# Performance work log

Measured on AMD Instinct MI355X. Metric: run time of the kernel, lower is better.

The kernel has to match this reference:

```python
import jax, jax.numpy as jnp
import numpy as np

N_NODES = 50000
N_EDGES = 1600000
NFEAT, NHID, NCLASS = 512, 128, 40


def setup_inputs() -> dict:
    key = jax.random.key(0)
    ks = jax.random.split(key, 10)
    x = jax.random.normal(ks[0], (N_NODES, NFEAT), dtype=jnp.float32)
    edge_src = jax.random.randint(ks[1], (N_EDGES,), 0, N_NODES, dtype=jnp.int32)
    edge_dst = jax.random.randint(ks[2], (N_EDGES,), 0, N_NODES, dtype=jnp.int32)
    edge_weight = jax.random.uniform(ks[3], (N_EDGES,), dtype=jnp.float32)
    # GraphConvolution params: gc1 (nfeat->nhid), one additional (nhid->nhid), gc2 (nhid->nclass)
    s1 = 1.0 / np.sqrt(NHID)
    s2 = 1.0 / np.sqrt(NCLASS)
    W1 = jax.random.uniform(ks[4], (NFEAT, NHID), minval=-s1, maxval=s1, dtype=jnp.float32)
    b1 = jax.random.uniform(ks[5], (NHID,), minval=-s1, maxval=s1, dtype=jnp.float32)
    Wh = jax.random.uniform(ks[6], (NHID, NHID), minval=-s1, maxval=s1, dtype=jnp.float32)
    bh = jax.random.uniform(ks[7], (NHID,), minval=-s1, maxval=s1, dtype=jnp.float32)
    W2 = jax.random.uniform(ks[8], (NHID, NCLASS), minval=-s2, maxval=s2, dtype=jnp.float32)
    b2 = jax.random.uniform(ks[9], (NCLASS,), minval=-s2, maxval=s2, dtype=jnp.float32)
    return {"x": x, "edge_src": edge_src, "edge_dst": edge_dst, "edge_weight": edge_weight,
            "W1": W1, "b1": b1, "Wh": Wh, "bh": bh, "W2": W2, "b2": b2}


def reference(x, edge_src, edge_dst, edge_weight, W1, b1, Wh, bh, W2, b2):
    def spmm(h):
        # out[i] = sum_j adj[i, j] * h[j]  with adj given as weighted edge list (src=j, dst=i)
        return jax.ops.segment_sum(edge_weight[:, None] * h[edge_src], edge_dst,
                                   num_segments=x.shape[0])

    def gconv(h, W, b):
        return spmm(h @ W) + b  # dense transform then sparse aggregation

    h = jax.nn.relu(gconv(x, W1, b1))       # gc1
    h = jax.nn.relu(gconv(h, Wh, bh))        # additional hidden layer
    h = gconv(h, W2, b2)                     # gc2
    return jax.nn.log_softmax(h, axis=1)
```

## Files before the change

### kernel.cpp

```cpp
#include <hip/hip_runtime.h>
#include <hip/hip_bf16.h>
#include <math.h>

#define N_NODES 50000
#define N_EDGES 1600000
#define NFEAT 512
#define NHID 128
#define NCLASS 40

#define NBUCKETS 196
#define BUCKET_CAP 16384

typedef __attribute__((ext_vector_type(8))) short bf16x8;
typedef __attribute__((ext_vector_type(4))) float f32x4;

static __device__ __forceinline__ float asfloat_u32(unsigned int u) {
    union { unsigned int u; float f; } c;
    c.u = u;
    return c.f;
}
static __device__ __forceinline__ unsigned int asu32_f(float f) {
    union { float f; unsigned int u; } c;
    c.f = f;
    return c.u;
}
static __device__ __forceinline__ unsigned short f2bf(float f) {
    union { float f; unsigned int u; } c;
    c.f = f;
    unsigned int r = c.u + 0x7FFFu + ((c.u >> 16) & 1u);
    return (unsigned short)(r >> 16);
}

__global__ __launch_bounds__(256) void prep_kernel(const float* __restrict__ W1,
                                                   unsigned short* __restrict__ Wt1,
                                                   const float* __restrict__ Wh,
                                                   unsigned short* __restrict__ Wth,
                                                   int* __restrict__ bucketCursor) {
    int idx = blockIdx.x * 256 + threadIdx.x;
    if (idx < NFEAT * NHID) {
        int k = idx >> 7;
        int n = idx & 127;
        Wt1[(size_t)n * NFEAT + k] = f2bf(W1[idx]);
    } else if (idx < NFEAT * NHID + NHID * NHID) {
        int j = idx - NFEAT * NHID;
        int k = j >> 7;
        int n = j & 127;
        Wth[(size_t)n * NHID + k] = f2bf(Wh[j]);
    } else {
        int j = idx - (NFEAT * NHID + NHID * NHID);
        if (j < NBUCKETS) bucketCursor[j] = j * BUCKET_CAP;
    }
}

#define LDP 40
#define GEMM_LDS_BYTES ((64 + 128) * LDP * 2)

template <bool A_IS_BF16>
static __device__ __forceinline__ void gemm64_body(const void* __restrict__ Ap,
                                                   const unsigned short* __restrict__ Wt,
                                                   unsigned short* __restrict__ C,
                                                   const int M, const int K,
                                                   char* smem, int bid) {
    unsigned short* As = (unsigned short*)smem;
    unsigned short* Bs = (unsigned short*)smem + 64 * LDP;
    const int tid = threadIdx.x;
    const int wave = tid >> 6;
    const int lane = tid & 63;
    const int ln = lane & 15;
    const int quad = lane >> 4;
    const int row0 = bid * 64;

    const int ar = tid >> 2;
    const int ac = (tid & 3) * 8;
    const bool arOk = (row0 + ar) < M;
    const int bn = tid >> 1;
    const int bk = (tid & 1) * 16;

    f32x4 acc[8];
#pragma unroll
    for (int t = 0; t < 8; ++t) acc[t] = (f32x4){0.f, 0.f, 0.f, 0.f};

    for (int kc = 0; kc < K; kc += 32) {
        bf16x8 va;
        if (A_IS_BF16) {
            if (arOk) {
                va = *(const bf16x8*)((const unsigned short*)Ap +
                                      (size_t)(row0 + ar) * K + kc + ac);
            } else {
#pragma unroll
                for (int i = 0; i < 8; ++i) va[i] = 0;
            }
        } else {
            if (arOk) {
                const float* Af = (const float*)Ap + (size_t)(row0 + ar) * K + kc + ac;
                float4 f0 = *(const float4*)(Af);
                float4 f1 = *(const float4*)(Af + 4);
                va[0] = (short)f2bf(f0.x); va[1] = (short)f2bf(f0.y);
                va[2] = (short)f2bf(f0.z); va[3] = (short)f2bf(f0.w);
                va[4] = (short)f2bf(f1.x); va[5] = (short)f2bf(f1.y);
                va[6] = (short)f2bf(f1.z); va[7] = (short)f2bf(f1.w);
            } else {
#pragma unroll
                for (int i = 0; i < 8; ++i) va[i] = 0;
            }
        }
        const unsigned short* Bg = Wt + (size_t)bn * K + kc + bk;
        bf16x8 vb0 = *(const bf16x8*)Bg;
        bf16x8 vb1 = *(const bf16x8*)(Bg + 8);

        __syncthreads();
        *(bf16x8*)&As[ar * LDP + ac] = va;
        *(bf16x8*)&Bs[bn * LDP + bk] = vb0;
        *(bf16x8*)&Bs[bn * LDP + bk + 8] = vb1;
        __syncthreads();

        bf16x8 a = *(const bf16x8*)&As[(wave * 16 + ln) * LDP + quad * 8];
#pragma unroll
        for (int t = 0; t < 8; ++t) {
            bf16x8 b = *(const bf16x8*)&Bs[(t * 16 + ln) * LDP + quad * 8];
            acc[t] = __builtin_amdgcn_mfma_f32_16x16x32_bf16(a, b, acc[t], 0, 0, 0);
        }
    }

#pragma unroll
    for (int t = 0; t < 8; ++t) {
#pragma unroll
        for (int r = 0; r < 4; ++r) {
            int row = row0 + wave * 16 + quad * 4 + r;
            if (row < M) C[(size_t)row * 128 + t * 16 + ln] = f2bf(acc[t][r]);
        }
    }
}

static __device__ __forceinline__ void bin_body(const int* __restrict__ src,
                                                const int* __restrict__ dst,
                                                const float* __restrict__ w,
                                                int* __restrict__ bucketCursor,
                                                uint2* __restrict__ binned,
                                                int n, char* smem, int bid) {
    int* hist = (int*)smem;
    int* cur = (int*)smem + NBUCKETS;
    const int tid = threadIdx.x;
    const int base = bid * 4096;
    if (tid < NBUCKETS) hist[tid] = 0;
    __syncthreads();
#pragma unroll
    for (int r = 0; r < 16; ++r) {
        int e = base + r * 256 + tid;
        if (e < n) atomicAdd(&hist[dst[e] >> 8], 1);
    }
    __syncthreads();
    if (tid < NBUCKETS && hist[tid] > 0)
        cur[tid] = atomicAdd(&bucketCursor[tid], hist[tid]);
    __syncthreads();
#pragma unroll
    for (int r = 0; r < 16; ++r) {
        int e = base + r * 256 + tid;
        if (e < n) {
            int d = dst[e];
            int pos = atomicAdd(&cur[d >> 8], 1);
            uint2 rec;
            rec.x = (unsigned int)src[e] | ((unsigned int)(d & 255) << 16);
            rec.y = asu32_f(w[e]);
            binned[pos] = rec;
        }
    }
}

#define GEMM1_BLOCKS 782
#define BIN_BLOCKS 391
__global__ __launch_bounds__(256) void fused_gemm1_bin(const float* __restrict__ x,
                                                       const unsigned short* __restrict__ Wt1,
                                                       unsigned short* __restrict__ tb,
                                                       const int* __restrict__ src,
                                                       const int* __restrict__ dst,
                                                       const float* __restrict__ w,
                                                       int* __restrict__ bucketCursor,
                                                       uint2* __restrict__ binned) {
    __shared__ char smem[GEMM_LDS_BYTES];
    if (blockIdx.x < GEMM1_BLOCKS) {
        gemm64_body<false>(x, Wt1, tb, N_NODES, NFEAT, smem, blockIdx.x);
    } else {
        bin_body(src, dst, w, bucketCursor, binned, N_EDGES, smem,
                 blockIdx.x - GEMM1_BLOCKS);
    }
}

__global__ __launch_bounds__(256) void gemm64_l2(const unsigned short* __restrict__ A,
                                                 const unsigned short* __restrict__ Wt,
                                                 unsigned short* __restrict__ C) {
    __shared__ char smem[GEMM_LDS_BYTES];
    gemm64_body<true>(A, Wt, C, N_NODES, NHID, smem, blockIdx.x);
}

__global__ __launch_bounds__(256) void build_csr(const uint2* __restrict__ binned,
                                                 const int* __restrict__ bucketCursor,
                                                 unsigned int* __restrict__ pairs,
                                                 int* __restrict__ row_ptr) {
    __shared__ int bs[256];
    __shared__ int hist[256];
    __shared__ int sc[256];
    __shared__ int cur[256];
    const int b = blockIdx.x;
    const int tid = threadIdx.x;

    int c = (tid < NBUCKETS) ? (bucketCursor[tid] - tid * BUCKET_CAP) : 0;
    bs[tid] = c;
    __syncthreads();
    for (int off = 1; off < 256; off <<= 1) {
        int t = (tid >= off) ? bs[tid - off] : 0;
        __syncthreads();
        bs[tid] += t;
        __syncthreads();
    }
    const int cnt = bucketCursor[b] - b * BUCKET_CAP;
    const int segStart = bs[b] - cnt;
    if (b == NBUCKETS - 1 && tid == 0) row_ptr[N_NODES] = bs[NBUCKETS - 1];
    const uint2* seg = binned + (size_t)b * BUCKET_CAP;

    hist[tid] = 0;
    __syncthreads();
    for (int i = tid; i < cnt; i += 256)
        atomicAdd(&hist[seg[i].x >> 16], 1);
    __syncthreads();
    int v = hist[tid];
    sc[tid] = v;
    __syncthreads();
    for (int off = 1; off < 256; off <<= 1) {
        int t = (tid >= off) ? sc[tid - off] : 0;
        __syncthreads();
        sc[tid] += t;
        __syncthreads();
    }
    int excl = sc[tid] - v;
    int node = b * 256 + tid;
    if (node < N_NODES) row_ptr[node] = segStart + excl;
    cur[tid] = segStart + excl;
    __syncthreads();
    for (int i = tid; i < cnt; i += 256) {
        uint2 p = seg[i];
        int pos = atomicAdd(&cur[p.x >> 16], 1);
        pairs[pos] = (p.x & 0xFFFFu) | ((unsigned int)f2bf(asfloat_u32(p.y)) << 16);
    }
}

__global__ __launch_bounds__(256) void gemm_n40_bf16A(const unsigned short* __restrict__ A,
                                                      const float* __restrict__ Bm,
                                                      unsigned short* __restrict__ C, int M) {
    __shared__ float As[64][132];
    __shared__ float Bs[128 * 40];
    const int tid = threadIdx.x;
    const int tr = tid >> 2;
    const int tc = tid & 3;
    const int row0 = blockIdx.x * 64;

#pragma unroll
    for (int q = tid; q < 2048; q += 256) {
        int r = q >> 5;
        int c = (q & 31) << 2;
        int row = row0 + r;
        uint2 u = make_uint2(0u, 0u);
        if (row < M) u = *(const uint2*)(A + (size_t)row * 128 + c);
        As[r][c + 0] = asfloat_u32(u.x << 16);
        As[r][c + 1] = asfloat_u32(u.x & 0xFFFF0000u);
        As[r][c + 2] = asfloat_u32(u.y << 16);
        As[r][c + 3] = asfloat_u32(u.y & 0xFFFF0000u);
    }
    for (int q = tid; q < 128 * 40; q += 256) Bs[q] = Bm[q];
    __syncthreads();

    float acc[10];
#pragma unroll
    for (int j = 0; j < 10; ++j) acc[j] = 0.f;

    for (int k = 0; k < 128; ++k) {
        float a = As[tr][k];
#pragma unroll
        for (int j = 0; j < 10; ++j) acc[j] += a * Bs[k * 40 + tc * 10 + j];
    }

    int row = row0 + tr;
    if (row < M) {
#pragma unroll
        for (int j = 0; j < 10; ++j) C[(size_t)row * 40 + tc * 10 + j] = f2bf(acc[j]);
    }
}

__global__ __launch_bounds__(256) void spmm_bias_relu_bf16(const unsigned short* __restrict__ t,
                                                           const int* __restrict__ row_ptr,
                                                           const unsigned int* __restrict__ pairs,
                                                           const float* __restrict__ bias,
                                                           unsigned short* __restrict__ out) {
    const int node = blockIdx.x * 4 + (threadIdx.x >> 6);
    const int lane = threadIdx.x & 63;
    const int e0 = row_ptr[node];
    const int e1 = row_ptr[node + 1];
    float ax = 0.f, ay = 0.f;
    int e = e0;
    for (; e + 8 <= e1; e += 8) {
        unsigned int p0 = pairs[e],     p1 = pairs[e + 1], p2 = pairs[e + 2], p3 = pairs[e + 3];
        unsigned int p4 = pairs[e + 4], p5 = pairs[e + 5], p6 = pairs[e + 6], p7 = pairs[e + 7];
        unsigned int v0 = *(const unsigned int*)(t + (size_t)(p0 & 0xFFFFu) * 128 + lane * 2);
        unsigned int v1 = *(const unsigned int*)(t + (size_t)(p1 & 0xFFFFu) * 128 + lane * 2);
        unsigned int v2 = *(const unsigned int*)(t + (size_t)(p2 & 0xFFFFu) * 128 + lane * 2);
        unsigned int v3 = *(const unsigned int*)(t + (size_t)(p3 & 0xFFFFu) * 128 + lane * 2);
        unsigned int v4 = *(const unsigned int*)(t + (size_t)(p4 & 0xFFFFu) * 128 + lane * 2);
        unsigned int v5 = *(const unsigned int*)(t + (size_t)(p5 & 0xFFFFu) * 128 + lane * 2);
        unsigned int v6 = *(const unsigned int*)(t + (size_t)(p6 & 0xFFFFu) * 128 + lane * 2);
        unsigned int v7 = *(const unsigned int*)(t + (size_t)(p7 & 0xFFFFu) * 128 + lane * 2);
        float w0 = asfloat_u32(p0 & 0xFFFF0000u), w1 = asfloat_u32(p1 & 0xFFFF0000u);
        float w2 = asfloat_u32(p2 & 0xFFFF0000u), w3 = asfloat_u32(p3 & 0xFFFF0000u);
        float w4 = asfloat_u32(p4 & 0xFFFF0000u), w5 = asfloat_u32(p5 & 0xFFFF0000u);
        float w6 = asfloat_u32(p6 & 0xFFFF0000u), w7 = asfloat_u32(p7 & 0xFFFF0000u);
        ax += w0 * asfloat_u32(v0 << 16); ay += w0 * asfloat_u32(v0 & 0xFFFF0000u);
        ax += w1 * asfloat_u32(v1 << 16); ay += w1 * asfloat_u32(v1 & 0xFFFF0000u);
        ax += w2 * asfloat_u32(v2 << 16); ay += w2 * asfloat_u32(v2 & 0xFFFF0000u);
        ax += w3 * asfloat_u32(v3 << 16); ay += w3 * asfloat_u32(v3 & 0xFFFF0000u);
        ax += w4 * asfloat_u32(v4 << 16); ay += w4 * asfloat_u32(v4 & 0xFFFF0000u);
        ax += w5 * asfloat_u32(v5 << 16); ay += w5 * asfloat_u32(v5 & 0xFFFF0000u);
        ax += w6 * asfloat_u32(v6 << 16); ay += w6 * asfloat_u32(v6 & 0xFFFF0000u);
        ax += w7 * asfloat_u32(v7 << 16); ay += w7 * asfloat_u32(v7 & 0xFFFF0000u);
    }
    for (; e < e1; ++e) {
        unsigned int p = pairs[e];
        float w = asfloat_u32(p & 0xFFFF0000u);
        unsigned int v = *(const unsigned int*)(t + (size_t)(p & 0xFFFFu) * 128 + lane * 2);
        ax += w * asfloat_u32(v << 16);
        ay += w * asfloat_u32(v & 0xFFFF0000u);
    }
    float2 b = *(const float2*)&bias[lane * 2];
    ax = fmaxf(ax + b.x, 0.f);
    ay = fmaxf(ay + b.y, 0.f);
    unsigned int packed = ((unsigned int)f2bf(ax)) | (((unsigned int)f2bf(ay)) << 16);
    *(unsigned int*)(out + (size_t)node * 128 + lane * 2) = packed;
}

__global__ __launch_bounds__(256) void spmm_logsoftmax(const unsigned short* __restrict__ t,
                                                       const int* __restrict__ row_ptr,
                                                       const unsigned int* __restrict__ pairs,
                                                       const float* __restrict__ bias,
                                                       float* __restrict__ out) {
    const int node = blockIdx.x * 4 + (threadIdx.x >> 6);
    const int lane = threadIdx.x & 63;
    const int e0 = row_ptr[node];
    const int e1 = row_ptr[node + 1];
    const bool act = lane < NCLASS;
    float acc = 0.f;
    int e = e0;
    for (; e + 4 <= e1; e += 4) {
        unsigned int p0 = pairs[e], p1 = pairs[e + 1], p2 = pairs[e + 2], p3 = pairs[e + 3];
        if (act) {
            float v0 = asfloat_u32((unsigned int)t[(size_t)(p0 & 0xFFFFu) * NCLASS + lane] << 16);
            float v1 = asfloat_u32((unsigned int)t[(size_t)(p1 & 0xFFFFu) * NCLASS + lane] << 16);
            float v2 = asfloat_u32((unsigned int)t[(size_t)(p2 & 0xFFFFu) * NCLASS + lane] << 16);
            float v3 = asfloat_u32((unsigned int)t[(size_t)(p3 & 0xFFFFu) * NCLASS + lane] << 16);
            acc += asfloat_u32(p0 & 0xFFFF0000u) * v0 + asfloat_u32(p1 & 0xFFFF0000u) * v1 +
                   asfloat_u32(p2 & 0xFFFF0000u) * v2 + asfloat_u32(p3 & 0xFFFF0000u) * v3;
        }
    }
    for (; e < e1; ++e) {
        unsigned int p = pairs[e];
        if (act)
            acc += asfloat_u32(p & 0xFFFF0000u) *
                   asfloat_u32((unsigned int)t[(size_t)(p & 0xFFFFu) * NCLASS + lane] << 16);
    }
    float logit = act ? (acc + bias[lane]) : -INFINITY;
    float m = logit;
#pragma unroll
    for (int off = 32; off; off >>= 1) m = fmaxf(m, __shfl_xor(m, off));
    float ex = act ? __expf(logit - m) : 0.f;
    float ssum = ex;
#pragma unroll
    for (int off = 32; off; off >>= 1) ssum += __shfl_xor(ssum, off);
    if (act) out[(size_t)node * NCLASS + lane] = logit - m - __logf(ssum);
}


extern "C" void kernel_launch(void* const* d_in, const int* in_sizes, int n_in,
                              void* d_out, int out_size, void* d_ws, size_t ws_size,
                              hipStream_t stream) {
    const float* x = (const float*)d_in[0];
    const int* edge_src = (const int*)d_in[1];
    const int* edge_dst = (const int*)d_in[2];
    const float* edge_weight = (const float*)d_in[3];
    const float* W1 = (const float*)d_in[4];
    const float* b1 = (const float*)d_in[5];
    const float* Wh = (const float*)d_in[6];
    const float* bh = (const float*)d_in[7];
    const float* W2 = (const float*)d_in[8];
    const float* b2 = (const float*)d_in[9];
    float* out = (float*)d_out;

    size_t off = 0;
    auto carve = [&](size_t bytes) {
        void* p = (char*)d_ws + off;
        off += (bytes + 511) & ~(size_t)511;
        return p;
    };
    unsigned short* tb = (unsigned short*)carve((size_t)N_NODES * 128 * 2);
    unsigned short* hb = (unsigned short*)carve((size_t)N_NODES * 128 * 2);
    unsigned short* t3 = (unsigned short*)carve((size_t)N_NODES * NCLASS * 2);
    unsigned short* Wt1 = (unsigned short*)carve((size_t)NFEAT * NHID * 2);
    unsigned short* Wth = (unsigned short*)carve((size_t)NHID * NHID * 2);
    int* row_ptr = (int*)carve((size_t)(N_NODES + 4) * 4);
    int* bucketCursor = (int*)carve((size_t)NBUCKETS * 4);
    uint2* binned = (uint2*)carve((size_t)NBUCKETS * BUCKET_CAP * 8);
    unsigned int* pairs = (unsigned int*)carve((size_t)N_EDGES * 4);
    (void)ws_size; (void)n_in; (void)in_sizes; (void)out_size;

    const int prepBlocks = (NFEAT * NHID + NHID * NHID + NBUCKETS + 255) / 256;
    const int spmmBlocks = N_NODES / 4;
    const int gemmBlocks = (N_NODES + 63) / 64;

    prep_kernel<<<prepBlocks, 256, 0, stream>>>(W1, Wt1, Wh, Wth, bucketCursor);

    fused_gemm1_bin<<<GEMM1_BLOCKS + BIN_BLOCKS, 256, 0, stream>>>(
        x, Wt1, tb, edge_src, edge_dst, edge_weight, bucketCursor, binned);

    build_csr<<<NBUCKETS, 256, 0, stream>>>(binned, bucketCursor, pairs, row_ptr);

    spmm_bias_relu_bf16<<<spmmBlocks, 256, 0, stream>>>(tb, row_ptr, pairs, b1, hb);

    gemm64_l2<<<gemmBlocks, 256, 0, stream>>>(hb, Wth, tb);
    spmm_bias_relu_bf16<<<spmmBlocks, 256, 0, stream>>>(tb, row_ptr, pairs, bh, hb);

    gemm_n40_bf16A<<<gemmBlocks, 256, 0, stream>>>(hb, W2, t3, N_NODES);
    spmm_logsoftmax<<<spmmBlocks, 256, 0, stream>>>(t3, row_ptr, pairs, b2, out);
}
```

Measured before the change: 437.1 us.

## Double-buffer GEMM global loads and split SpMM edges across half-waves

The 64-row MFMA GEMM now keeps two register stages of global loads in flight, issuing the load for tile k+2 before computing tile k, so global latency overlaps the MFMAs. The hidden-layer SpMM splits each node's edges between the two half-waves, with each lane gathering 8 bytes (4 bf16 features) per edge, and then combines the halves with a cross-lane shuffle. The intent is more memory parallelism per wave and wider gathers, at the cost of extra registers and a reduction step. The GEMM loop assumes K/32 is even.

```diff
diff --git a/kernel.cpp b/kernel.cpp
--- a/kernel.cpp
+++ b/kernel.cpp
@@ -76,51 +76,87 @@
     const int bn = tid >> 1;
     const int bk = (tid & 1) * 16;
 
+    const unsigned short* Abf = (const unsigned short*)Ap + (size_t)(row0 + ar) * K + ac;
+    const float* Af = (const float*)Ap + (size_t)(row0 + ar) * K + ac;
+    const unsigned short* Bg = Wt + (size_t)bn * K + bk;
+
     f32x4 acc[8];
 #pragma unroll
     for (int t = 0; t < 8; ++t) acc[t] = (f32x4){0.f, 0.f, 0.f, 0.f};
 
-    for (int kc = 0; kc < K; kc += 32) {
-        bf16x8 va;
-        if (A_IS_BF16) {
-            if (arOk) {
-                va = *(const bf16x8*)((const unsigned short*)Ap +
-                                      (size_t)(row0 + ar) * K + kc + ac);
-            } else {
-#pragma unroll
-                for (int i = 0; i < 8; ++i) va[i] = 0;
-            }
-        } else {
-            if (arOk) {
-                const float* Af = (const float*)Ap + (size_t)(row0 + ar) * K + kc + ac;
-                float4 f0 = *(const float4*)(Af);
-                float4 f1 = *(const float4*)(Af + 4);
-                va[0] = (short)f2bf(f0.x); va[1] = (short)f2bf(f0.y);
-                va[2] = (short)f2bf(f0.z); va[3] = (short)f2bf(f0.w);
-                va[4] = (short)f2bf(f1.x); va[5] = (short)f2bf(f1.y);
-                va[6] = (short)f2bf(f1.z); va[7] = (short)f2bf(f1.w);
-            } else {
-#pragma unroll
-                for (int i = 0; i < 8; ++i) va[i] = 0;
-            }
-        }
-        const unsigned short* Bg = Wt + (size_t)bn * K + kc + bk;
-        bf16x8 vb0 = *(const bf16x8*)Bg;
-        bf16x8 vb1 = *(const bf16x8*)(Bg + 8);
-
-        __syncthreads();
-        *(bf16x8*)&As[ar * LDP + ac] = va;
-        *(bf16x8*)&Bs[bn * LDP + bk] = vb0;
-        *(bf16x8*)&Bs[bn * LDP + bk + 8] = vb1;
-        __syncthreads();
-
-        bf16x8 a = *(const bf16x8*)&As[(wave * 16 + ln) * LDP + quad * 8];
-#pragma unroll
-        for (int t = 0; t < 8; ++t) {
-            bf16x8 b = *(const bf16x8*)&Bs[(t * 16 + ln) * LDP + quad * 8];
-            acc[t] = __builtin_amdgcn_mfma_f32_16x16x32_bf16(a, b, acc[t], 0, 0, 0);
-        }
-    }
+    const int NK = K >> 5;
+
+    bf16x8 vaA, vaB;
+    float4 faA0, faA1, faB0, faB1;
+    bf16x8 vb0A, vb1A, vb0B, vb1B;
+
+#define G64_ISSUE(kc, va_, fa0_, fa1_, vb0_, vb1_)                         \
+    do {                                                                   \
+        if (A_IS_BF16) {                                                   \
+            if (arOk) va_ = *(const bf16x8*)(Abf + (kc));                  \
+        } else {                                                           \
+            if (arOk) {                                                    \
+                fa0_ = *(const float4*)(Af + (kc));                        \
+                fa1_ = *(const float4*)(Af + (kc) + 4);                    \
+            }                                                              \
+        }                                                                  \
+        vb0_ = *(const bf16x8*)(Bg + (kc));                                \
+        vb1_ = *(const bf16x8*)(Bg + (kc) + 8);                            \
+    } while (0)
+
+#define G64_STAGE(va_, fa0_, fa1_, vb0_, vb1_)                             \
+    do {                                                                   \
+        bf16x8 vw;                                                         \
+        if (A_IS_BF16) {                                                   \
+            if (arOk) {                                                    \
+                vw = va_;                                                  \
+            } else {                                                       \
+                _Pragma("unroll") for (int i = 0; i < 8; ++i) vw[i] = 0;   \
+            }                                                              \
+        } else {                                                           \
+            if (arOk) {                                                    \
+                vw[0] = (short)f2bf(fa0_.x); vw[1] = (short)f2bf(fa0_.y);  \
+                vw[2] = (short)f2bf(fa0_.z); vw[3] = (short)f2bf(fa0_.w);  \
+                vw[4] = (short)f2bf(fa1_.x); vw[5] = (short)f2bf(fa1_.y);  \
+                vw[6] = (short)f2bf(fa1_.z); vw[7] = (short)f2bf(fa1_.w);  \
+            } else {                                                       \
+                _Pragma("unroll") for (int i = 0; i < 8; ++i) vw[i] = 0;   \
+            }                                                              \
+        }                                                                  \
+        *(bf16x8*)&As[ar * LDP + ac] = vw;                                 \
+        *(bf16x8*)&Bs[bn * LDP + bk] = vb0_;                               \
+        *(bf16x8*)&Bs[bn * LDP + bk + 8] = vb1_;                           \
+    } while (0)
+
+#define G64_COMPUTE()                                                          \
+    do {                                                                       \
+        bf16x8 a = *(const bf16x8*)&As[(wave * 16 + ln) * LDP + quad * 8];     \
+        _Pragma("unroll") for (int t = 0; t < 8; ++t) {                        \
+            bf16x8 b = *(const bf16x8*)&Bs[(t * 16 + ln) * LDP + quad * 8];    \
+            acc[t] = __builtin_amdgcn_mfma_f32_16x16x32_bf16(a, b, acc[t], 0, 0, 0); \
+        }                                                                      \
+    } while (0)
+
+    G64_ISSUE(0, vaA, faA0, faA1, vb0A, vb1A);
+    G64_ISSUE(32, vaB, faB0, faB1, vb0B, vb1B);
+
+    for (int it = 0; it < NK; it += 2) {
+        __syncthreads();
+        G64_STAGE(vaA, faA0, faA1, vb0A, vb1A);
+        __syncthreads();
+        if (it + 2 < NK) G64_ISSUE((it + 2) * 32, vaA, faA0, faA1, vb0A, vb1A);
+        G64_COMPUTE();
+
+        __syncthreads();
+        G64_STAGE(vaB, faB0, faB1, vb0B, vb1B);
+        __syncthreads();
+        if (it + 3 < NK) G64_ISSUE((it + 3) * 32, vaB, faB0, faB1, vb0B, vb1B);
+        G64_COMPUTE();
+    }
+
+#undef G64_ISSUE
+#undef G64_STAGE
+#undef G64_COMPUTE
 
 #pragma unroll
     for (int t = 0; t < 8; ++t) {
@@ -293,46 +329,62 @@
                                                            unsigned short* __restrict__ out) {
     const int node = blockIdx.x * 4 + (threadIdx.x >> 6);
     const int lane = threadIdx.x & 63;
+    const int half = lane >> 5;
+    const int fq = (lane & 31) * 4;
     const int e0 = row_ptr[node];
     const int e1 = row_ptr[node + 1];
-    float ax = 0.f, ay = 0.f;
+    float a0 = 0.f, a1 = 0.f, a2 = 0.f, a3 = 0.f;
     int e = e0;
-    for (; e + 8 <= e1; e += 8) {
-        unsigned int p0 = pairs[e],     p1 = pairs[e + 1], p2 = pairs[e + 2], p3 = pairs[e + 3];
-        unsigned int p4 = pairs[e + 4], p5 = pairs[e + 5], p6 = pairs[e + 6], p7 = pairs[e + 7];
-        unsigned int v0 = *(const unsigned int*)(t + (size_t)(p0 & 0xFFFFu) * 128 + lane * 2);
-        unsigned int v1 = *(const unsigned int*)(t + (size_t)(p1 & 0xFFFFu) * 128 + lane * 2);
-        unsigned int v2 = *(const unsigned int*)(t + (size_t)(p2 & 0xFFFFu) * 128 + lane * 2);
-        unsigned int v3 = *(const unsigned int*)(t + (size_t)(p3 & 0xFFFFu) * 128 + lane * 2);
-        unsigned int v4 = *(const unsigned int*)(t + (size_t)(p4 & 0xFFFFu) * 128 + lane * 2);
-        unsigned int v5 = *(const unsigned int*)(t + (size_t)(p5 & 0xFFFFu) * 128 + lane * 2);
-        unsigned int v6 = *(const unsigned int*)(t + (size_t)(p6 & 0xFFFFu) * 128 + lane * 2);
-        unsigned int v7 = *(const unsigned int*)(t + (size_t)(p7 & 0xFFFFu) * 128 + lane * 2);
-        float w0 = asfloat_u32(p0 & 0xFFFF0000u), w1 = asfloat_u32(p1 & 0xFFFF0000u);
-        float w2 = asfloat_u32(p2 & 0xFFFF0000u), w3 = asfloat_u32(p3 & 0xFFFF0000u);
-        float w4 = asfloat_u32(p4 & 0xFFFF0000u), w5 = asfloat_u32(p5 & 0xFFFF0000u);
-        float w6 = asfloat_u32(p6 & 0xFFFF0000u), w7 = asfloat_u32(p7 & 0xFFFF0000u);
-        ax += w0 * asfloat_u32(v0 << 16); ay += w0 * asfloat_u32(v0 & 0xFFFF0000u);
-        ax += w1 * asfloat_u32(v1 << 16); ay += w1 * asfloat_u32(v1 & 0xFFFF0000u);
-        ax += w2 * asfloat_u32(v2 << 16); ay += w2 * asfloat_u32(v2 & 0xFFFF0000u);
-        ax += w3 * asfloat_u32(v3 << 16); ay += w3 * asfloat_u32(v3 & 0xFFFF0000u);
-        ax += w4 * asfloat_u32(v4 << 16); ay += w4 * asfloat_u32(v4 & 0xFFFF0000u);
-        ax += w5 * asfloat_u32(v5 << 16); ay += w5 * asfloat_u32(v5 & 0xFFFF0000u);
-        ax += w6 * asfloat_u32(v6 << 16); ay += w6 * asfloat_u32(v6 & 0xFFFF0000u);
-        ax += w7 * asfloat_u32(v7 << 16); ay += w7 * asfloat_u32(v7 & 0xFFFF0000u);
-    }
-    for (; e < e1; ++e) {
+    for (; e + 16 <= e1; e += 16) {
+        unsigned int p[8];
+        uint2 v[8];
+#pragma unroll
+        for (int i = 0; i < 8; ++i) p[i] = pairs[e + 2 * i + half];
+#pragma unroll
+        for (int i = 0; i < 8; ++i)
+            v[i] = *(const uint2*)(t + (size_t)(p[i] & 0xFFFFu) * 128 + fq);
+#pragma unroll
+        for (int i = 0; i < 8; ++i) {
+            float w = asfloat_u32(p[i] & 0xFFFF0000u);
+            a0 += w * asfloat_u32(v[i].x << 16);
+            a1 += w * asfloat_u32(v[i].x & 0xFFFF0000u);
+            a2 += w * asfloat_u32(v[i].y << 16);
+            a3 += w * asfloat_u32(v[i].y & 0xFFFF0000u);
+        }
+    }
+    for (; e + 2 <= e1; e += 2) {
+        unsigned int p = pairs[e + half];
+        uint2 v = *(const uint2*)(t + (size_t)(p & 0xFFFFu) * 128 + fq);
+        float w = asfloat_u32(p & 0xFFFF0000u);
+        a0 += w * asfloat_u32(v.x << 16);
+        a1 += w * asfloat_u32(v.x & 0xFFFF0000u);
+        a2 += w * asfloat_u32(v.y << 16);
+        a3 += w * asfloat_u32(v.y & 0xFFFF0000u);
+    }
+    if (e < e1 && half == 0) {
         unsigned int p = pairs[e];
+        uint2 v = *(const uint2*)(t + (size_t)(p & 0xFFFFu) * 128 + fq);
         float w = asfloat_u32(p & 0xFFFF0000u);
-        unsigned int v = *(const unsigned int*)(t + (size_t)(p & 0xFFFFu) * 128 + lane * 2);
-        ax += w * asfloat_u32(v << 16);
-        ay += w * asfloat_u32(v & 0xFFFF0000u);
-    }
-    float2 b = *(const float2*)&bias[lane * 2];
-    ax = fmaxf(ax + b.x, 0.f);
-    ay = fmaxf(ay + b.y, 0.f);
-    unsigned int packed = ((unsigned int)f2bf(ax)) | (((unsigned int)f2bf(ay)) << 16);
-    *(unsigned int*)(out + (size_t)node * 128 + lane * 2) = packed;
+        a0 += w * asfloat_u32(v.x << 16);
+        a1 += w * asfloat_u32(v.x & 0xFFFF0000u);
+        a2 += w * asfloat_u32(v.y << 16);
+        a3 += w * asfloat_u32(v.y & 0xFFFF0000u);
+    }
+    a0 += __shfl_xor(a0, 32);
+    a1 += __shfl_xor(a1, 32);
+    a2 += __shfl_xor(a2, 32);
+    a3 += __shfl_xor(a3, 32);
+    if (half == 0) {
+        float4 b = *(const float4*)&bias[fq];
+        a0 = fmaxf(a0 + b.x, 0.f);
+        a1 = fmaxf(a1 + b.y, 0.f);
+        a2 = fmaxf(a2 + b.z, 0.f);
+        a3 = fmaxf(a3 + b.w, 0.f);
+        uint2 o;
+        o.x = ((unsigned int)f2bf(a0)) | (((unsigned int)f2bf(a1)) << 16);
+        o.y = ((unsigned int)f2bf(a2)) | (((unsigned int)f2bf(a3)) << 16);
+        *(uint2*)(out + (size_t)node * 128 + fq) = o;
+    }
 }
 
 __global__ __launch_bounds__(256) void spmm_logsoftmax(const unsigned short* __restrict__ t,
```

Measured after the change: 436.1 us. About the same (-0.2%).
